# Performance work log

Hardware: AMD Instinct MI355X
Metric: run time of the kernel (lower is better)

## Reference

```python
import jax, jax.numpy as jnp
import numpy as np

GROUP_SIZE = 128
TOP_K = 2
ZERO_POINT = 8  # Marlin symmetric zero point: w = scale * (q - 8)


def _dequant_int4(q, scales, group_size):
    # q: [E, N, K] int values in [0,15]; scales: [E, N, K//group_size]
    s = jnp.repeat(scales, group_size, axis=-1)  # [E, N, K]
    return (q.astype(jnp.float32) - float(ZERO_POINT)) * s


def setup_inputs() -> dict:
    key = jax.random.key(0)
    k1, k2, k3, k4, k5, k6 = jax.random.split(key, 6)
    B, S, H, I, E = 2, 1024, 2048, 1408, 8
    router_logits = jax.random.normal(k1, (B, S, E), dtype=jnp.float32)
    hidden_states = jax.random.normal(k2, (B, S, H), dtype=jnp.float32)
    fc_gate_up_qweights = jax.random.randint(k3, (E, 2 * I, H), 0, 16, dtype=jnp.int32)
    fc_gate_up_scales = jax.random.uniform(k4, (E, 2 * I, H // GROUP_SIZE), dtype=jnp.float32) * 0.02
    fc_down_qweights = jax.random.randint(k5, (E, H, I), 0, 16, dtype=jnp.int32)
    fc_down_scales = jax.random.uniform(k6, (E, H, I // GROUP_SIZE), dtype=jnp.float32) * 0.02
    return {
        "router_logits": router_logits,
        "hidden_states": hidden_states,
        "fc_gate_up_qweights": fc_gate_up_qweights,
        "fc_gate_up_scales": fc_gate_up_scales,
        "fc_down_qweights": fc_down_qweights,
        "fc_down_scales": fc_down_scales,
    }


def reference(router_logits, hidden_states, fc_gate_up_qweights, fc_gate_up_scales,
              fc_down_qweights, fc_down_scales):
    B, S, H = hidden_states.shape
    E = router_logits.shape[-1]
    T = B * S
    x = hidden_states.reshape(T, H)
    logits = router_logits.reshape(T, E)

    # top-k routing with softmax over selected logits
    top_vals, top_idx = jax.lax.top_k(logits, TOP_K)          # [T, k]
    top_w = jax.nn.softmax(top_vals, axis=-1)                 # [T, k]
    route_w = jnp.zeros((T, E), x.dtype).at[jnp.arange(T)[:, None], top_idx].set(top_w)  # [T, E]

    # dequantize int4 weights: scale * (q - 8), per-group along K
    w_gate_up = _dequant_int4(fc_gate_up_qweights, fc_gate_up_scales, GROUP_SIZE)  # [E, 2I, H]
    w_down = _dequant_int4(fc_down_qweights, fc_down_scales, GROUP_SIZE)          # [E, H, I]

    # grouped GEMM (dense over experts, masked by routing weights)
    gu = jnp.einsum('th,enh->ten', x, w_gate_up)              # [T, E, 2I]
    gate, up = jnp.split(gu, 2, axis=-1)
    act = jax.nn.silu(gate) * up                              # SwiGLU, [T, E, I]
    out = jnp.einsum('tei,ehi,te->th', act, w_down, route_w)  # [T, H]
    return out.reshape(B, S, H)
```

## Files before the change

### kernel.cpp

```cpp
#include <hip/hip_runtime.h>
#include <hip/hip_bf16.h>

#define T_TOKENS 2048
#define H_DIM    2048
#define I_DIM    1408
#define E_NUM    8

typedef __bf16 bf16;
typedef __attribute__((ext_vector_type(8))) __bf16  bf16x8;
typedef __attribute__((ext_vector_type(4))) float   floatx4;

static const size_t OFF_COUNTS = 0;
static const size_t OFF_LISTS  = 256;
static const size_t OFF_WLISTS = OFF_LISTS + (size_t)T_TOKENS * E_NUM * 4;
static const size_t OFF_XB     = 131328;
static const size_t OFF_ACT    = OFF_XB + (size_t)T_TOKENS * H_DIM * 2;
static const size_t OFF_GUPK   = OFF_ACT + (size_t)2 * T_TOKENS * I_DIM * 2;
static const size_t OFF_DNPK   = OFF_GUPK + (size_t)E_NUM * 22 * 32 * 16384;

__device__ __forceinline__ void gload_lds16(const bf16* g, bf16* l)
{
    __builtin_amdgcn_global_load_lds((const __attribute__((address_space(1))) void*)g,
                                     (__attribute__((address_space(3))) void*)l,
                                     16, 0, 0);
}

__global__ __launch_bounds__(256) void pack_gu_kernel(const int* __restrict__ q,
                                                      const float* __restrict__ sc,
                                                      bf16* __restrict__ out)
{
    const int b = blockIdx.x;
    const int t = threadIdx.x;
    const int e = b / 2816;
    const int grow = b - e * 2816;
    const int4* qp = reinterpret_cast<const int4*>(q + (size_t)b * H_DIM) + t * 2;
    int4 a = qp[0], c = qp[1];
    float s = sc[(size_t)b * 16 + (t >> 4)];
    float m8s = -8.f * s;
    bf16x8 bv;
    bv[0] = (bf16)fmaf((float)a.x, s, m8s);
    bv[1] = (bf16)fmaf((float)a.y, s, m8s);
    bv[2] = (bf16)fmaf((float)a.z, s, m8s);
    bv[3] = (bf16)fmaf((float)a.w, s, m8s);
    bv[4] = (bf16)fmaf((float)c.x, s, m8s);
    bv[5] = (bf16)fmaf((float)c.y, s, m8s);
    bv[6] = (bf16)fmaf((float)c.z, s, m8s);
    bv[7] = (bf16)fmaf((float)c.w, s, m8s);
    const int is_up = grow >= I_DIM;
    const int icol  = grow - (is_up ? I_DIM : 0);
    const int nt    = icol >> 6;
    const int r     = ((((icol >> 4) & 3) * 2 + is_up) * 16) + (icol & 15);
    size_t dst = ((((size_t)e * 22 + nt) * 32 + (t >> 3)) * 128 + r) * 8 + ((t & 7) ^ (r & 7));
    reinterpret_cast<bf16x8*>(out)[dst] = bv;
}

__global__ __launch_bounds__(256) void pack_dn_kernel(const int* __restrict__ q,
                                                      const float* __restrict__ sc,
                                                      bf16* __restrict__ out)
{
    const int b = blockIdx.x;
    const int t = threadIdx.x;
    if (t >= 176) return;
    const int e = b >> 11;
    const int grow = b & 2047;
    const int4* qp = reinterpret_cast<const int4*>(q + (size_t)b * I_DIM) + t * 2;
    int4 a = qp[0], c = qp[1];
    float s = sc[(size_t)b * 11 + (t >> 4)];
    float m8s = -8.f * s;
    bf16x8 bv;
    bv[0] = (bf16)fmaf((float)a.x, s, m8s);
    bv[1] = (bf16)fmaf((float)a.y, s, m8s);
    bv[2] = (bf16)fmaf((float)a.z, s, m8s);
    bv[3] = (bf16)fmaf((float)a.w, s, m8s);
    bv[4] = (bf16)fmaf((float)c.x, s, m8s);
    bv[5] = (bf16)fmaf((float)c.y, s, m8s);
    bv[6] = (bf16)fmaf((float)c.z, s, m8s);
    bv[7] = (bf16)fmaf((float)c.w, s, m8s);
    const int nt = grow >> 7;
    const int r  = grow & 127;
    size_t dst = ((((size_t)e * 16 + nt) * 22 + (t >> 3)) * 128 + r) * 8 + ((t & 7) ^ (r & 7));
    reinterpret_cast<bf16x8*>(out)[dst] = bv;
}

__global__ void xconv_kernel(const float* __restrict__ x, bf16* __restrict__ xb)
{
    int i = blockIdx.x * blockDim.x + threadIdx.x;
    const float4* x4 = reinterpret_cast<const float4*>(x) + (size_t)i * 2;
    float4 v0 = x4[0], v1 = x4[1];
    bf16x8 bv;
    bv[0] = (bf16)v0.x; bv[1] = (bf16)v0.y; bv[2] = (bf16)v0.z; bv[3] = (bf16)v0.w;
    bv[4] = (bf16)v1.x; bv[5] = (bf16)v1.y; bv[6] = (bf16)v1.z; bv[7] = (bf16)v1.w;
    *reinterpret_cast<bf16x8*>(xb + (size_t)i * 8) = bv;
}

__global__ void router_kernel(const float* __restrict__ logits,
                              int* __restrict__ counts,
                              int* __restrict__ lists,
                              float* __restrict__ wlists)
{
    int t = blockIdx.x * blockDim.x + threadIdx.x;
    if (t >= T_TOKENS) return;
    const float* l = logits + (size_t)t * E_NUM;
    float v0 = -1e30f, v1 = -1e30f;
    int i0 = 0, i1 = 0;
    #pragma unroll
    for (int e = 0; e < E_NUM; ++e) {
        float v = l[e];
        if (v > v0) { v1 = v0; i1 = i0; v0 = v; i0 = e; }
        else if (v > v1) { v1 = v; i1 = e; }
    }
    float w0 = 1.f / (1.f + __expf(v1 - v0));
    float w1 = 1.f - w0;
    int p0 = atomicAdd(&counts[i0], 1);
    lists[i0 * T_TOKENS + p0] = t * 2 + 0;
    wlists[i0 * T_TOKENS + p0] = w0;
    int p1 = atomicAdd(&counts[i1], 1);
    lists[i1 * T_TOKENS + p1] = t * 2 + 1;
    wlists[i1 * T_TOKENS + p1] = w1;
}

__global__ __launch_bounds__(256) void gemm1_kernel(
    const bf16* __restrict__ xb,
    const bf16* __restrict__ wpk,
    const int*  __restrict__ counts,
    const int*  __restrict__ lists,
    bf16*       __restrict__ act)
{
    const int lid = (blockIdx.x & 7) * 352 + (blockIdx.x >> 3);
    const int e   = lid / 352;
    const int r_  = lid - e * 352;
    const int nt  = r_ >> 4;
    const int m0  = (r_ & 15) * 128;
    const int cnt = counts[e];
    if (m0 >= cnt) return;

    __shared__ __align__(16) bf16 Al[8192];
    __shared__ __align__(16) bf16 Bl[8192];
    __shared__ int meta[128];

    const int tid = threadIdx.x;
    if (tid < 128) {
        int m = m0 + tid;
        meta[tid] = lists[e * T_TOKENS + (m < cnt ? m : 0)];
    }
    __syncthreads();

    const int lane = tid & 63;
    const int wv = tid >> 6;
    const int wm = wv >> 1, wn = wv & 1;

    size_t agbl[4];
    #pragma unroll
    for (int j = 0; j < 4; ++j) {
        int g = tid + 256 * j;
        int arow = g >> 3, cg = g & 7;
        agbl[j] = (size_t)(meta[arow] >> 1) * H_DIM + ((cg ^ (arow & 7)) * 8);
    }
    const bf16* bt = wpk + ((size_t)e * 22 + nt) * (32 * 8192) + tid * 8;

    int afr[2][4], bfr[2][4];
    #pragma unroll
    for (int ks = 0; ks < 2; ++ks) {
        int gidx = ks * 4 + (lane >> 4);
        #pragma unroll
        for (int t4 = 0; t4 < 4; ++t4) {
            int ra = wm * 64 + t4 * 16 + (lane & 15);
            afr[ks][t4] = ra * 64 + ((gidx ^ (ra & 7)) * 8);
            int rb = wn * 64 + t4 * 16 + (lane & 15);
            bfr[ks][t4] = rb * 64 + ((gidx ^ (rb & 7)) * 8);
        }
    }

    floatx4 acc[4][4];
    #pragma unroll
    for (int i = 0; i < 4; ++i)
        #pragma unroll
        for (int j = 0; j < 4; ++j)
            acc[i][j] = (floatx4){0.f, 0.f, 0.f, 0.f};

    for (int k0 = 0; k0 < H_DIM; k0 += 64) {
        #pragma unroll
        for (int j = 0; j < 4; ++j)
            gload_lds16(xb + agbl[j] + k0, &Al[(tid + 256 * j) * 8]);
        const bf16* bsrc = bt + (size_t)(k0 >> 6) * 8192;
        #pragma unroll
        for (int j = 0; j < 4; ++j)
            gload_lds16(bsrc + j * 2048, &Bl[tid * 8 + j * 2048]);
        __syncthreads();
        #pragma unroll
        for (int ks = 0; ks < 2; ++ks) {
            bf16x8 af[4], bff[4];
            #pragma unroll
            for (int mt = 0; mt < 4; ++mt)
                af[mt] = *reinterpret_cast<const bf16x8*>(&Al[afr[ks][mt]]);
            #pragma unroll
            for (int ntf = 0; ntf < 4; ++ntf)
                bff[ntf] = *reinterpret_cast<const bf16x8*>(&Bl[bfr[ks][ntf]]);
            #pragma unroll
            for (int mt = 0; mt < 4; ++mt)
                #pragma unroll
                for (int ntf = 0; ntf < 4; ++ntf)
                    acc[mt][ntf] = __builtin_amdgcn_mfma_f32_16x16x32_bf16(af[mt], bff[ntf], acc[mt][ntf], 0, 0, 0);
        }
        __syncthreads();
    }

    const int rbase = (lane >> 4) * 4;
    const int cn = lane & 15;
    #pragma unroll
    for (int mt = 0; mt < 4; ++mt) {
        #pragma unroll
        for (int j = 0; j < 2; ++j) {
            floatx4 g = acc[mt][2 * j];
            floatx4 u = acc[mt][2 * j + 1];
            int col = nt * 64 + (wn * 2 + j) * 16 + cn;
            #pragma unroll
            for (int r = 0; r < 4; ++r) {
                int lrow = wm * 64 + mt * 16 + rbase + r;
                if (m0 + lrow < cnt) {
                    float gate = g[r], up = u[r];
                    float a = gate / (1.f + __expf(-gate)) * up;
                    act[(size_t)meta[lrow] * I_DIM + col] = (bf16)a;
                }
            }
        }
    }
}

__global__ __launch_bounds__(256) void gemm2_kernel(
    const bf16*  __restrict__ act,
    const bf16*  __restrict__ wpk,
    const int*   __restrict__ counts,
    const int*   __restrict__ lists,
    const float* __restrict__ wlists,
    float*       __restrict__ out)
{
    const int lid = (blockIdx.x & 7) * 256 + (blockIdx.x >> 3);
    const int e   = lid >> 8;
    const int r_  = lid & 255;
    const int nt  = r_ >> 4;
    const int m0  = (r_ & 15) * 128;
    const int cnt = counts[e];
    if (m0 >= cnt) return;

    __shared__ __align__(16) bf16 Al[8192];
    __shared__ __align__(16) bf16 Bl[8192];
    __shared__ int   meta[128];
    __shared__ float wmeta[128];

    const int tid = threadIdx.x;
    if (tid < 128) {
        int m = m0 + tid;
        int mm = (m < cnt) ? m : 0;
        meta[tid]  = lists[e * T_TOKENS + mm];
        wmeta[tid] = wlists[e * T_TOKENS + mm];
    }
    __syncthreads();

    const int lane = tid & 63;
    const int wv = tid >> 6;
    const int wm = wv >> 1, wn = wv & 1;

    size_t agbl[4];
    #pragma unroll
    for (int j = 0; j < 4; ++j) {
        int g = tid + 256 * j;
        int arow = g >> 3, cg = g & 7;
        agbl[j] = (size_t)meta[arow] * I_DIM + ((cg ^ (arow & 7)) * 8);
    }
    const bf16* bt = wpk + ((size_t)e * 16 + nt) * (22 * 8192) + tid * 8;

    int afr[2][4], bfr[2][4];
    #pragma unroll
    for (int ks = 0; ks < 2; ++ks) {
        int gidx = ks * 4 + (lane >> 4);
        #pragma unroll
        for (int t4 = 0; t4 < 4; ++t4) {
            int ra = wm * 64 + t4 * 16 + (lane & 15);
            afr[ks][t4] = ra * 64 + ((gidx ^ (ra & 7)) * 8);
            int rb = wn * 64 + t4 * 16 + (lane & 15);
            bfr[ks][t4] = rb * 64 + ((gidx ^ (rb & 7)) * 8);
        }
    }

    floatx4 acc[4][4];
    #pragma unroll
    for (int i = 0; i < 4; ++i)
        #pragma unroll
        for (int j = 0; j < 4; ++j)
            acc[i][j] = (floatx4){0.f, 0.f, 0.f, 0.f};

    for (int kt = 0; kt < 22; ++kt) {
        #pragma unroll
        for (int j = 0; j < 4; ++j)
            gload_lds16(act + agbl[j] + kt * 64, &Al[(tid + 256 * j) * 8]);
        const bf16* bsrc = bt + (size_t)kt * 8192;
        #pragma unroll
        for (int j = 0; j < 4; ++j)
            gload_lds16(bsrc + j * 2048, &Bl[tid * 8 + j * 2048]);
        __syncthreads();
        #pragma unroll
        for (int ks = 0; ks < 2; ++ks) {
            bf16x8 af[4], bff[4];
            #pragma unroll
            for (int mt = 0; mt < 4; ++mt)
                af[mt] = *reinterpret_cast<const bf16x8*>(&Al[afr[ks][mt]]);
            #pragma unroll
            for (int ntf = 0; ntf < 4; ++ntf)
                bff[ntf] = *reinterpret_cast<const bf16x8*>(&Bl[bfr[ks][ntf]]);
            #pragma unroll
            for (int mt = 0; mt < 4; ++mt)
                #pragma unroll
                for (int ntf = 0; ntf < 4; ++ntf)
                    acc[mt][ntf] = __builtin_amdgcn_mfma_f32_16x16x32_bf16(af[mt], bff[ntf], acc[mt][ntf], 0, 0, 0);
        }
        __syncthreads();
    }

    const int rbase = (lane >> 4) * 4;
    const int cn = lane & 15;
    #pragma unroll
    for (int mt = 0; mt < 4; ++mt) {
        #pragma unroll
        for (int ntf = 0; ntf < 4; ++ntf) {
            floatx4 v = acc[mt][ntf];
            int col = nt * 128 + wn * 64 + ntf * 16 + cn;
            #pragma unroll
            for (int r = 0; r < 4; ++r) {
                int lrow = wm * 64 + mt * 16 + rbase + r;
                if (m0 + lrow < cnt) {
                    int tok = meta[lrow] >> 1;
                    atomicAdd(&out[(size_t)tok * H_DIM + col], wmeta[lrow] * v[r]);
                }
            }
        }
    }
}

extern "C" void kernel_launch(void* const* d_in, const int* in_sizes, int n_in,
                              void* d_out, int out_size, void* d_ws, size_t ws_size,
                              hipStream_t stream)
{
    const float* router_logits = (const float*)d_in[0];
    const float* x             = (const float*)d_in[1];
    const int*   gu_q          = (const int*)d_in[2];
    const float* gu_s          = (const float*)d_in[3];
    const int*   dn_q          = (const int*)d_in[4];
    const float* dn_s          = (const float*)d_in[5];
    float* out = (float*)d_out;

    char* ws = (char*)d_ws;
    int*   counts = (int*)(ws + OFF_COUNTS);
    int*   lists  = (int*)(ws + OFF_LISTS);
    float* wlists = (float*)(ws + OFF_WLISTS);
    bf16*  xb     = (bf16*)(ws + OFF_XB);
    bf16*  act    = (bf16*)(ws + OFF_ACT);
    bf16*  gu_pk  = (bf16*)(ws + OFF_GUPK);
    bf16*  dn_pk  = (bf16*)(ws + OFF_DNPK);

    hipMemsetAsync(counts, 0, E_NUM * sizeof(int), stream);
    hipMemsetAsync(out, 0, (size_t)T_TOKENS * H_DIM * sizeof(float), stream);

    pack_gu_kernel<<<E_NUM * 2816, 256, 0, stream>>>(gu_q, gu_s, gu_pk);
    pack_dn_kernel<<<E_NUM * 2048, 256, 0, stream>>>(dn_q, dn_s, dn_pk);
    xconv_kernel<<<T_TOKENS * H_DIM / 8 / 256, 256, 0, stream>>>(x, xb);
    router_kernel<<<T_TOKENS / 256, 256, 0, stream>>>(router_logits, counts, lists, wlists);

    gemm1_kernel<<<22 * 16 * E_NUM, 256, 0, stream>>>(xb, gu_pk, counts, lists, act);
    gemm2_kernel<<<16 * 16 * E_NUM, 256, 0, stream>>>(act, dn_pk, counts, lists, wlists, out);
}
```

Before: 544.4 us.

## Pack weight tiles with contiguous writes and replace output atomics with slot buffer

The int4-to-bf16 pack kernels now assign one block per output tile. Each block gathers its rows from the source and writes the packed tile contiguously, instead of reading one source row and scattering 16-byte writes across tiles. The down-projection GEMM no longer atomically accumulates into a zeroed output. It writes each token's weighted expert-slot result to a temporary buffer that reuses the gate/up packed-weight region, and a new finalize kernel sums the two slots. This removes the output memset and the atomic contention, at the cost of extra temporary-buffer traffic and one more kernel launch.

Result: no change. 544.2 us (-0.1%).

```diff
diff --git a/kernel.cpp b/kernel.cpp
--- a/kernel.cpp
+++ b/kernel.cpp
@@ -17,6 +17,7 @@
 static const size_t OFF_ACT    = OFF_XB + (size_t)T_TOKENS * H_DIM * 2;
 static const size_t OFF_GUPK   = OFF_ACT + (size_t)2 * T_TOKENS * I_DIM * 2;
 static const size_t OFF_DNPK   = OFF_GUPK + (size_t)E_NUM * 22 * 32 * 16384;
+static const size_t OFF_TMP    = OFF_GUPK;
 
 __device__ __forceinline__ void gload_lds16(const bf16* g, bf16* l)
 {
@@ -29,57 +30,71 @@
                                                       const float* __restrict__ sc,
                                                       bf16* __restrict__ out)
 {
-    const int b = blockIdx.x;
-    const int t = threadIdx.x;
-    const int e = b / 2816;
-    const int grow = b - e * 2816;
-    const int4* qp = reinterpret_cast<const int4*>(q + (size_t)b * H_DIM) + t * 2;
-    int4 a = qp[0], c = qp[1];
-    float s = sc[(size_t)b * 16 + (t >> 4)];
-    float m8s = -8.f * s;
-    bf16x8 bv;
-    bv[0] = (bf16)fmaf((float)a.x, s, m8s);
-    bv[1] = (bf16)fmaf((float)a.y, s, m8s);
-    bv[2] = (bf16)fmaf((float)a.z, s, m8s);
-    bv[3] = (bf16)fmaf((float)a.w, s, m8s);
-    bv[4] = (bf16)fmaf((float)c.x, s, m8s);
-    bv[5] = (bf16)fmaf((float)c.y, s, m8s);
-    bv[6] = (bf16)fmaf((float)c.z, s, m8s);
-    bv[7] = (bf16)fmaf((float)c.w, s, m8s);
-    const int is_up = grow >= I_DIM;
-    const int icol  = grow - (is_up ? I_DIM : 0);
-    const int nt    = icol >> 6;
-    const int r     = ((((icol >> 4) & 3) * 2 + is_up) * 16) + (icol & 15);
-    size_t dst = ((((size_t)e * 22 + nt) * 32 + (t >> 3)) * 128 + r) * 8 + ((t & 7) ^ (r & 7));
-    reinterpret_cast<bf16x8*>(out)[dst] = bv;
+    const int bid = blockIdx.x;
+    const int kt  = bid & 31;
+    const int en  = bid >> 5;
+    const int nt  = en % 22;
+    const int e   = en / 22;
+    const int tid = threadIdx.x;
+    bf16x8* ob = reinterpret_cast<bf16x8*>(out) + (size_t)bid * 1024;
+    #pragma unroll
+    for (int j = 0; j < 4; ++j) {
+        const int s     = tid + 256 * j;
+        const int r     = s >> 3;
+        const int gl    = (s & 7) ^ (r & 7);
+        const int p2    = r >> 4;
+        const int is_up = p2 & 1;
+        const int icol  = nt * 64 + (p2 >> 1) * 16 + (r & 15);
+        const size_t row_q = (size_t)e * 2816 + (is_up ? I_DIM : 0) + icol;
+        const int4* qp = reinterpret_cast<const int4*>(q + row_q * H_DIM + kt * 64 + gl * 8);
+        int4 a = qp[0], c = qp[1];
+        float sv = sc[row_q * 16 + (kt >> 1)];
+        float m8 = -8.f * sv;
+        bf16x8 bv;
+        bv[0] = (bf16)fmaf((float)a.x, sv, m8);
+        bv[1] = (bf16)fmaf((float)a.y, sv, m8);
+        bv[2] = (bf16)fmaf((float)a.z, sv, m8);
+        bv[3] = (bf16)fmaf((float)a.w, sv, m8);
+        bv[4] = (bf16)fmaf((float)c.x, sv, m8);
+        bv[5] = (bf16)fmaf((float)c.y, sv, m8);
+        bv[6] = (bf16)fmaf((float)c.z, sv, m8);
+        bv[7] = (bf16)fmaf((float)c.w, sv, m8);
+        ob[s] = bv;
+    }
 }
 
 __global__ __launch_bounds__(256) void pack_dn_kernel(const int* __restrict__ q,
                                                       const float* __restrict__ sc,
                                                       bf16* __restrict__ out)
 {
-    const int b = blockIdx.x;
-    const int t = threadIdx.x;
-    if (t >= 176) return;
-    const int e = b >> 11;
-    const int grow = b & 2047;
-    const int4* qp = reinterpret_cast<const int4*>(q + (size_t)b * I_DIM) + t * 2;
-    int4 a = qp[0], c = qp[1];
-    float s = sc[(size_t)b * 11 + (t >> 4)];
-    float m8s = -8.f * s;
-    bf16x8 bv;
-    bv[0] = (bf16)fmaf((float)a.x, s, m8s);
-    bv[1] = (bf16)fmaf((float)a.y, s, m8s);
-    bv[2] = (bf16)fmaf((float)a.z, s, m8s);
-    bv[3] = (bf16)fmaf((float)a.w, s, m8s);
-    bv[4] = (bf16)fmaf((float)c.x, s, m8s);
-    bv[5] = (bf16)fmaf((float)c.y, s, m8s);
-    bv[6] = (bf16)fmaf((float)c.z, s, m8s);
-    bv[7] = (bf16)fmaf((float)c.w, s, m8s);
-    const int nt = grow >> 7;
-    const int r  = grow & 127;
-    size_t dst = ((((size_t)e * 16 + nt) * 22 + (t >> 3)) * 128 + r) * 8 + ((t & 7) ^ (r & 7));
-    reinterpret_cast<bf16x8*>(out)[dst] = bv;
+    const int bid = blockIdx.x;
+    const int kt  = bid % 22;
+    const int en  = bid / 22;
+    const int nt  = en & 15;
+    const int e   = en >> 4;
+    const int tid = threadIdx.x;
+    bf16x8* ob = reinterpret_cast<bf16x8*>(out) + (size_t)bid * 1024;
+    #pragma unroll
+    for (int j = 0; j < 4; ++j) {
+        const int s  = tid + 256 * j;
+        const int r  = s >> 3;
+        const int gl = (s & 7) ^ (r & 7);
+        const size_t row_q = (size_t)e * 2048 + nt * 128 + r;
+        const int4* qp = reinterpret_cast<const int4*>(q + row_q * I_DIM + kt * 64 + gl * 8);
+        int4 a = qp[0], c = qp[1];
+        float sv = sc[row_q * 11 + (kt >> 1)];
+        float m8 = -8.f * sv;
+        bf16x8 bv;
+        bv[0] = (bf16)fmaf((float)a.x, sv, m8);
+        bv[1] = (bf16)fmaf((float)a.y, sv, m8);
+        bv[2] = (bf16)fmaf((float)a.z, sv, m8);
+        bv[3] = (bf16)fmaf((float)a.w, sv, m8);
+        bv[4] = (bf16)fmaf((float)c.x, sv, m8);
+        bv[5] = (bf16)fmaf((float)c.y, sv, m8);
+        bv[6] = (bf16)fmaf((float)c.z, sv, m8);
+        bv[7] = (bf16)fmaf((float)c.w, sv, m8);
+        ob[s] = bv;
+    }
 }
 
 __global__ void xconv_kernel(const float* __restrict__ x, bf16* __restrict__ xb)
@@ -233,7 +248,7 @@
     const int*   __restrict__ counts,
     const int*   __restrict__ lists,
     const float* __restrict__ wlists,
-    float*       __restrict__ out)
+    float*       __restrict__ tmp)
 {
     const int lid = (blockIdx.x & 7) * 256 + (blockIdx.x >> 3);
     const int e   = lid >> 8;
@@ -329,12 +344,23 @@
             for (int r = 0; r < 4; ++r) {
                 int lrow = wm * 64 + mt * 16 + rbase + r;
                 if (m0 + lrow < cnt) {
-                    int tok = meta[lrow] >> 1;
-                    atomicAdd(&out[(size_t)tok * H_DIM + col], wmeta[lrow] * v[r]);
+                    tmp[(size_t)meta[lrow] * H_DIM + col] = wmeta[lrow] * v[r];
                 }
             }
         }
     }
+}
+
+__global__ void finalize_kernel(const float* __restrict__ tmp, float* __restrict__ out)
+{
+    int i4 = blockIdx.x * blockDim.x + threadIdx.x;
+    int t  = i4 >> 9;
+    int h  = (i4 & 511) * 4;
+    float4 a = *reinterpret_cast<const float4*>(tmp + ((size_t)2 * t) * H_DIM + h);
+    float4 b = *reinterpret_cast<const float4*>(tmp + ((size_t)(2 * t + 1)) * H_DIM + h);
+    float4 o;
+    o.x = a.x + b.x; o.y = a.y + b.y; o.z = a.z + b.z; o.w = a.w + b.w;
+    *reinterpret_cast<float4*>(out + (size_t)t * H_DIM + h) = o;
 }
 
 extern "C" void kernel_launch(void* const* d_in, const int* in_sizes, int n_in,
@@ -357,15 +383,16 @@
     bf16*  act    = (bf16*)(ws + OFF_ACT);
     bf16*  gu_pk  = (bf16*)(ws + OFF_GUPK);
     bf16*  dn_pk  = (bf16*)(ws + OFF_DNPK);
+    float* tmp    = (float*)(ws + OFF_TMP);
 
     hipMemsetAsync(counts, 0, E_NUM * sizeof(int), stream);
-    hipMemsetAsync(out, 0, (size_t)T_TOKENS * H_DIM * sizeof(float), stream);
-
-    pack_gu_kernel<<<E_NUM * 2816, 256, 0, stream>>>(gu_q, gu_s, gu_pk);
-    pack_dn_kernel<<<E_NUM * 2048, 256, 0, stream>>>(dn_q, dn_s, dn_pk);
+
+    pack_gu_kernel<<<E_NUM * 22 * 32, 256, 0, stream>>>(gu_q, gu_s, gu_pk);
+    pack_dn_kernel<<<E_NUM * 16 * 22, 256, 0, stream>>>(dn_q, dn_s, dn_pk);
     xconv_kernel<<<T_TOKENS * H_DIM / 8 / 256, 256, 0, stream>>>(x, xb);
     router_kernel<<<T_TOKENS / 256, 256, 0, stream>>>(router_logits, counts, lists, wlists);
 
     gemm1_kernel<<<22 * 16 * E_NUM, 256, 0, stream>>>(xb, gu_pk, counts, lists, act);
-    gemm2_kernel<<<16 * 16 * E_NUM, 256, 0, stream>>>(act, dn_pk, counts, lists, wlists, out);
-}
+    gemm2_kernel<<<16 * 16 * E_NUM, 256, 0, stream>>>(act, dn_pk, counts, lists, wlists, tmp);
+    finalize_kernel<<<4096, 256, 0, stream>>>(tmp, out);
+}
```
